# Kernel optimization log

Measured on AMD Instinct MI355X. Metric: run time of the kernel, lower is better.

The kernel has to match this reference:

```python
import jax, jax.numpy as jnp
import numpy as np

N_NODES = 100000
N_EDGES = 1600000
IN_DIM = 128
HID_DIM = 128
OUT_DIM = 2


def sage_conv(x, src, dst, deg_inv, W_l, W_r, b):
    # mean-aggregate neighbor features: messages flow src -> dst
    agg = jax.ops.segment_sum(x[src], dst, num_segments=N_NODES)  # [N, d_in]
    agg = agg * deg_inv[:, None]
    # PyG SAGEConv: out = lin_l(aggr) + lin_r(x); bias only on lin_l
    return agg @ W_l + x @ W_r + b


def setup_inputs() -> dict:
    key = jax.random.key(0)
    ks = jax.random.split(key, 9)
    x = jax.random.normal(ks[0], (N_NODES, IN_DIM), dtype=jnp.float32)
    edge_index = jax.random.randint(ks[1], (2, N_EDGES), 0, N_NODES, dtype=jnp.int64)

    def glorot(k, shape):
        lim = float(np.sqrt(6.0 / (shape[0] + shape[1])))
        return jax.random.uniform(k, shape, jnp.float32, -lim, lim)

    return {
        "x": x,
        "edge_index": edge_index,
        "W1_l": glorot(ks[2], (IN_DIM, HID_DIM)),
        "W1_r": glorot(ks[3], (IN_DIM, HID_DIM)),
        "b1": jnp.zeros((HID_DIM,), jnp.float32),
        "W2_l": glorot(ks[4], (HID_DIM, HID_DIM)),
        "W2_r": glorot(ks[5], (HID_DIM, HID_DIM)),
        "b2": jnp.zeros((HID_DIM,), jnp.float32),
        "W3_l": glorot(ks[6], (HID_DIM, OUT_DIM)),
        "W3_r": glorot(ks[7], (HID_DIM, OUT_DIM)),
        "b3": jnp.zeros((OUT_DIM,), jnp.float32),
    }


def reference(x, edge_index, W1_l, W1_r, b1, W2_l, W2_r, b2, W3_l, W3_r, b3):
    src, dst = edge_index[0], edge_index[1]
    # mean-aggregation normalization: 1/in-degree (clamped to >=1)
    deg = jax.ops.segment_sum(jnp.ones((N_EDGES,), jnp.float32), dst, num_segments=N_NODES)
    deg_inv = 1.0 / jnp.maximum(deg, 1.0)

    h = sage_conv(x, src, dst, deg_inv, W1_l, W1_r, b1)
    h = jax.nn.relu(h)  # dropout is identity in eval mode
    h = sage_conv(h, src, dst, deg_inv, W2_l, W2_r, b2)
    h = jax.nn.relu(h)
    h = sage_conv(h, src, dst, deg_inv, W3_l, W3_r, b3)
    h = jax.nn.relu(h)
    return jax.nn.log_softmax(h, axis=1)
```

## Files before the change

### kernel.cpp

```cpp
#include <hip/hip_runtime.h>
#include <hip/hip_bf16.h>
#include <math.h>

#define DIM 128

typedef __attribute__((ext_vector_type(8))) short bf16x8;
typedef __attribute__((ext_vector_type(4))) float f32x4;

__device__ __forceinline__ ushort f2bf(float f) {
  unsigned u = __float_as_uint(f);
  return (ushort)((u + 0x7FFFu + ((u >> 16) & 1u)) >> 16);
}
__device__ __forceinline__ float bf2f(ushort h) {
  return __uint_as_float(((unsigned)h) << 16);
}

__global__ __launch_bounds__(256) void prep_kernel(
    const int* __restrict__ dst, unsigned* __restrict__ deg, unsigned* __restrict__ rank, int E,
    const float* __restrict__ x, ushort* __restrict__ xh, long total,
    const float* __restrict__ W1l, const float* __restrict__ W1r,
    const float* __restrict__ W2l, const float* __restrict__ W2r,
    ushort* __restrict__ tabs, int H, int C) {
  const int bid = blockIdx.x;
  const int r = bid % 3;
  const int q = bid / 3;
  if (r == 0) {
    if (q < H) {
      int gid = q * 256 + threadIdx.x;
      if (gid < E) rank[gid] = atomicAdd(&deg[dst[gid]], 1u);
    }
    return;
  }
  int id2 = q * 2 + (r - 1);
  if (id2 < C) {
    long i = ((long)id2 * 256 + threadIdx.x) * 4;
    if (i >= total) return;
    float4 v = *(const float4*)(x + i);
    uint2 Hh;
    Hh.x = (unsigned)f2bf(v.x) | ((unsigned)f2bf(v.y) << 16);
    Hh.y = (unsigned)f2bf(v.z) | ((unsigned)f2bf(v.w) << 16);
    *(uint2*)(xh + i) = Hh;
    return;
  }
  id2 -= C;
  if (id2 >= 256) return;
  int m = id2 >> 6;
  const float* W = (m == 0) ? W1l : (m == 1) ? W1r : (m == 2) ? W2l : W2r;
  ushort* Ht = tabs + (size_t)m * 32768;
  ushort* Lt = Ht + 16384;
  int idx = (id2 & 63) * 256 + threadIdx.x;
  int k = idx >> 7, n = idx & 127;
  float v = W[idx];
  ushort h = f2bf(v);
  Ht[n * DIM + k] = h;
  Lt[n * DIM + k] = f2bf(v - bf2f(h));
}

__global__ __launch_bounds__(256) void scan_block_kernel(const unsigned* __restrict__ deg,
                                                         unsigned* __restrict__ excl,
                                                         unsigned* __restrict__ partial,
                                                         float* __restrict__ dinv, int N) {
  __shared__ unsigned s[256];
  int i = blockIdx.x * 256 + threadIdx.x;
  unsigned v = (i < N) ? deg[i] : 0u;
  if (i < N) dinv[i] = 1.0f / fmaxf((float)v, 1.0f);
  s[threadIdx.x] = v;
  __syncthreads();
#pragma unroll
  for (int d = 1; d < 256; d <<= 1) {
    unsigned t = (threadIdx.x >= d) ? s[threadIdx.x - d] : 0u;
    __syncthreads();
    s[threadIdx.x] += t;
    __syncthreads();
  }
  if (i < N) excl[i] = s[threadIdx.x] - v;
  if (threadIdx.x == 255) partial[blockIdx.x] = s[255];
}

__global__ __launch_bounds__(256) void scan_partials_kernel(unsigned* __restrict__ partial, int B) {
  __shared__ unsigned s[256];
  __shared__ unsigned carry;
  if (threadIdx.x == 0) carry = 0u;
  __syncthreads();
  for (int base = 0; base < B; base += 256) {
    int i = base + threadIdx.x;
    unsigned v = (i < B) ? partial[i] : 0u;
    s[threadIdx.x] = v;
    __syncthreads();
#pragma unroll
    for (int d = 1; d < 256; d <<= 1) {
      unsigned t = (threadIdx.x >= d) ? s[threadIdx.x - d] : 0u;
      __syncthreads();
      s[threadIdx.x] += t;
      __syncthreads();
    }
    if (i < B) partial[i] = carry + s[threadIdx.x] - v;
    __syncthreads();
    if (threadIdx.x == 0) carry += s[255];
    __syncthreads();
  }
}

__global__ __launch_bounds__(256) void add_offsets_kernel(const unsigned* __restrict__ excl,
                                                          const unsigned* __restrict__ partial,
                                                          unsigned* __restrict__ off, int N, int E) {
  int i = blockIdx.x * 256 + threadIdx.x;
  if (i < N) off[i] = excl[i] + partial[i >> 8];
  if (i == N) off[N] = (unsigned)E;
}

__global__ __launch_bounds__(256) void csr_fill_kernel(const int* __restrict__ src,
                                                       const int* __restrict__ dst,
                                                       const unsigned* __restrict__ rank,
                                                       const unsigned* __restrict__ off,
                                                       int* __restrict__ csr_src, int E) {
  int e = blockIdx.x * 256 + threadIdx.x;
  if (e >= E) return;
  csr_src[off[dst[e]] + rank[e]] = src[e];
}

__global__ __launch_bounds__(256) void gather_wave_kernel(
    const ushort* __restrict__ featH, const int* __restrict__ csr_src,
    const unsigned* __restrict__ off, const float* __restrict__ dinv,
    ushort* __restrict__ aggH, int N) {
  const int node = (blockIdx.x * 256 + threadIdx.x) >> 6;
  if (node >= N) return;
  const int lane = threadIdx.x & 63;
  const int eslot = lane >> 4;
  const int col = lane & 15;
  const unsigned beg = off[node], end = off[node + 1];
  const ushort* fbase = featH + col * 8;

  float acc[8];
#pragma unroll
  for (int t = 0; t < 8; ++t) acc[t] = 0.f;

  auto accum = [&](int4 v) {
    unsigned w0 = (unsigned)v.x, w1 = (unsigned)v.y, w2 = (unsigned)v.z, w3 = (unsigned)v.w;
    acc[0] += __uint_as_float(w0 << 16);
    acc[1] += __uint_as_float(w0 & 0xFFFF0000u);
    acc[2] += __uint_as_float(w1 << 16);
    acc[3] += __uint_as_float(w1 & 0xFFFF0000u);
    acc[4] += __uint_as_float(w2 << 16);
    acc[5] += __uint_as_float(w2 & 0xFFFF0000u);
    acc[6] += __uint_as_float(w3 << 16);
    acc[7] += __uint_as_float(w3 & 0xFFFF0000u);
  };

  unsigned base = beg;
  for (; base + 16 <= end; base += 16) {
    int s0 = csr_src[base + eslot];
    int s1 = csr_src[base + 4 + eslot];
    int s2 = csr_src[base + 8 + eslot];
    int s3 = csr_src[base + 12 + eslot];
    int4 v0 = *(const int4*)(fbase + (size_t)s0 * DIM);
    int4 v1 = *(const int4*)(fbase + (size_t)s1 * DIM);
    int4 v2 = *(const int4*)(fbase + (size_t)s2 * DIM);
    int4 v3 = *(const int4*)(fbase + (size_t)s3 * DIM);
    accum(v0); accum(v1); accum(v2); accum(v3);
  }
  for (; base + 8 <= end; base += 8) {
    int s0 = csr_src[base + eslot];
    int s1 = csr_src[base + 4 + eslot];
    int4 v0 = *(const int4*)(fbase + (size_t)s0 * DIM);
    int4 v1 = *(const int4*)(fbase + (size_t)s1 * DIM);
    accum(v0); accum(v1);
  }
  for (unsigned e = base + eslot; e < end; e += 4) {
    int s = csr_src[e];
    int4 v = *(const int4*)(fbase + (size_t)s * DIM);
    accum(v);
  }

#pragma unroll
  for (int t = 0; t < 8; ++t) {
    acc[t] += __shfl_xor(acc[t], 32, 64);
    acc[t] += __shfl_xor(acc[t], 16, 64);
  }

  if (eslot == 0) {
    float di = dinv[node];
    unsigned ph[4];
#pragma unroll
    for (int t = 0; t < 4; ++t) {
      ph[t] = (unsigned)f2bf(acc[2 * t] * di) | ((unsigned)f2bf(acc[2 * t + 1] * di) << 16);
    }
    *(int4*)(aggH + (size_t)node * DIM + col * 8) =
        make_int4((int)ph[0], (int)ph[1], (int)ph[2], (int)ph[3]);
  }
}

__global__ __launch_bounds__(256) void sage_mfma_kernel(
    const ushort* __restrict__ aggH, const ushort* xH,
    const ushort* __restrict__ WlH, const ushort* __restrict__ WlL,
    const ushort* __restrict__ WrH, const ushort* __restrict__ WrL,
    const float* __restrict__ bias,
    const float* __restrict__ W3l, const float* __restrict__ W3r,
    ushort* outH, float* __restrict__ y, int N) {
  __shared__ ushort As[128 * 64];
  __shared__ ushort Bs[2 * 128 * 64];

  const int tid = threadIdx.x;
  const int bm = blockIdx.x * 128;
  const int wave = tid >> 6;
  const int lane = tid & 63;
  const int l15 = lane & 15;
  const int quad = lane >> 4;
  const int wm = wave >> 1;
  const int wn = wave & 1;

  f32x4 acc[4][4];
#pragma unroll
  for (int i = 0; i < 4; ++i)
#pragma unroll
    for (int j = 0; j < 4; ++j) acc[i][j] = (f32x4){0.f, 0.f, 0.f, 0.f};

  for (int g = 0; g < 4; ++g) {
    const ushort* Ap = (g < 2) ? aggH : xH;
    const ushort* WH = (g < 2) ? WlH : WrH;
    const ushort* WL = (g < 2) ? WlL : WrL;
    const int kt = (g & 1) << 6;
    __syncthreads();
#pragma unroll
    for (int c = 0; c < 4; ++c) {
      int flat = c * 256 + tid;
      int row = flat >> 3;
      int kg = flat & 7;
      int swz = (kg ^ (row & 7)) << 3;
      int grow = bm + row;
      if (grow >= N) grow = N - 1;
      *(int4*)(&As[row * 64 + swz]) = *(const int4*)(Ap + (size_t)grow * DIM + kt + kg * 8);
    }
#pragma unroll
    for (int c = 0; c < 8; ++c) {
      int flat = c * 256 + tid;
      int tbl = flat >> 10;
      int row = (flat >> 3) & 127;
      int kg = flat & 7;
      int swz = (kg ^ (row & 7)) << 3;
      const ushort* Wp = tbl ? WL : WH;
      *(int4*)(&Bs[tbl * 8192 + row * 64 + swz]) =
          *(const int4*)(Wp + (size_t)row * DIM + kt + kg * 8);
    }
    __syncthreads();
#pragma unroll
    for (int ks = 0; ks < 2; ++ks) {
      bf16x8 af[4], bh[4], bl[4];
      int kg = (ks << 2) + quad;
#pragma unroll
      for (int i = 0; i < 4; ++i) {
        int ar = (wm << 6) + (i << 4) + l15;
        af[i] = *(const bf16x8*)(&As[ar * 64 + ((kg ^ (ar & 7)) << 3)]);
        int br = (wn << 6) + (i << 4) + l15;
        int bo = br * 64 + ((kg ^ (br & 7)) << 3);
        bh[i] = *(const bf16x8*)(&Bs[bo]);
        bl[i] = *(const bf16x8*)(&Bs[8192 + bo]);
      }
#pragma unroll
      for (int i = 0; i < 4; ++i)
#pragma unroll
        for (int j = 0; j < 4; ++j) {
          acc[i][j] = __builtin_amdgcn_mfma_f32_16x16x32_bf16(af[i], bh[j], acc[i][j], 0, 0, 0);
          acc[i][j] = __builtin_amdgcn_mfma_f32_16x16x32_bf16(af[i], bl[j], acc[i][j], 0, 0, 0);
        }
    }
  }

  __syncthreads();
  float* WcF = reinterpret_cast<float*>(As);
  float* YpF = reinterpret_cast<float*>(As) + 512;

  if (W3l) {
    for (int t = tid; t < 512; t += 256) {
      int col = t >> 2, c = t & 3;
      WcF[t] = (c < 2) ? W3l[col * 2 + c] : W3r[col * 2 + (c - 2)];
    }
    __syncthreads();
  }

  float bv[4];
#pragma unroll
  for (int j = 0; j < 4; ++j) bv[j] = bias[(wn << 6) + (j << 4) + l15];

#pragma unroll
  for (int i = 0; i < 4; ++i) {
#pragma unroll
    for (int r = 0; r < 4; ++r) {
      const int rowl = (wm << 6) + (i << 4) + (quad << 2) + r;
      const int grow = bm + rowl;
      float p0 = 0.f, p1 = 0.f, p2 = 0.f, p3 = 0.f;
#pragma unroll
      for (int j = 0; j < 4; ++j) {
        float v = fmaxf(acc[i][j][r] + bv[j], 0.f);
        ushort h = f2bf(v);
        if (grow < N) outH[(size_t)grow * DIM + (wn << 6) + (j << 4) + l15] = h;
        if (W3l) {
          float qv = bf2f(h);
          int col = (wn << 6) + (j << 4) + l15;
          p0 += qv * WcF[col * 4 + 0];
          p1 += qv * WcF[col * 4 + 1];
          p2 += qv * WcF[col * 4 + 2];
          p3 += qv * WcF[col * 4 + 3];
        }
      }
      if (W3l) {
#pragma unroll
        for (int o = 1; o < 16; o <<= 1) {
          p0 += __shfl_xor(p0, o, 64);
          p1 += __shfl_xor(p1, o, 64);
          p2 += __shfl_xor(p2, o, 64);
          p3 += __shfl_xor(p3, o, 64);
        }
        if (l15 == 0) {
          YpF[(rowl * 4 + 0) * 2 + wn] = p0;
          YpF[(rowl * 4 + 1) * 2 + wn] = p1;
          YpF[(rowl * 4 + 2) * 2 + wn] = p2;
          YpF[(rowl * 4 + 3) * 2 + wn] = p3;
        }
      }
    }
  }

  if (W3l) {
    __syncthreads();
    for (int t = tid; t < 512; t += 256) {
      int grow = bm + (t >> 2);
      if (grow < N) y[(size_t)grow * 4 + (t & 3)] = YpF[t * 2 + 0] + YpF[t * 2 + 1];
    }
  }
}

__global__ __launch_bounds__(256) void final3_kernel(const float* __restrict__ y,
                                                     const int* __restrict__ csr_src,
                                                     const unsigned* __restrict__ off,
                                                     const float* __restrict__ dinv,
                                                     const float* __restrict__ b3,
                                                     float* __restrict__ out, int N) {
  int n = blockIdx.x * 256 + threadIdx.x;
  if (n >= N) return;
  unsigned beg = off[n], end = off[n + 1];
  float s0 = 0.f, s1 = 0.f;
  for (unsigned e = beg; e < end; ++e) {
    int s = csr_src[e];
    float2 v = *reinterpret_cast<const float2*>(&y[(size_t)s * 4]);
    s0 += v.x; s1 += v.y;
  }
  float di = dinv[n];
  float o0 = fmaxf(s0 * di + y[(size_t)n * 4 + 2] + b3[0], 0.f);
  float o1 = fmaxf(s1 * di + y[(size_t)n * 4 + 3] + b3[1], 0.f);
  float m = fmaxf(o0, o1);
  float l = m + logf(expf(o0 - m) + expf(o1 - m));
  out[n * 2 + 0] = o0 - l;
  out[n * 2 + 1] = o1 - l;
}

extern "C" void kernel_launch(void* const* d_in, const int* in_sizes, int n_in,
                              void* d_out, int out_size, void* d_ws, size_t ws_size,
                              hipStream_t stream) {
  const float* x   = (const float*)d_in[0];
  const int*   ei  = (const int*)d_in[1];
  const float* W1l = (const float*)d_in[2];
  const float* W1r = (const float*)d_in[3];
  const float* b1  = (const float*)d_in[4];
  const float* W2l = (const float*)d_in[5];
  const float* W2r = (const float*)d_in[6];
  const float* b2  = (const float*)d_in[7];
  const float* W3l = (const float*)d_in[8];
  const float* W3r = (const float*)d_in[9];
  const float* b3  = (const float*)d_in[10];

  const int N = in_sizes[0] / DIM;
  const int E = in_sizes[1] / 2;
  const int* src = ei;
  const int* dst = ei + E;
  const int B = (N + 255) / 256;

  char* ws = (char*)d_ws;
  size_t off_b = 0;
  auto alloc = [&](size_t bytes) {
    void* p = ws + off_b;
    off_b = (off_b + bytes + 255) & ~(size_t)255;
    return p;
  };
  unsigned* deg     = (unsigned*)alloc((size_t)N * 4);
  unsigned* excl    = (unsigned*)alloc((size_t)N * 4);
  unsigned* partial = (unsigned*)alloc((size_t)B * 4);
  unsigned* offs    = (unsigned*)alloc((size_t)(N + 1) * 4);
  unsigned* rank    = (unsigned*)alloc((size_t)E * 4);
  int*      csr_src = (int*)alloc((size_t)E * 4);
  float*    dinv    = (float*)alloc((size_t)N * 4);
  ushort*   xH      = (ushort*)alloc((size_t)N * DIM * 2);
  ushort*   aggH    = (ushort*)alloc((size_t)N * DIM * 2);
  ushort*   wtabs   = (ushort*)alloc((size_t)8 * 16384 * 2);
  float*    y       = (float*)alloc((size_t)N * 4 * 4);

  const int H = (E + 255) / 256;
  const int C = (int)(((size_t)N * DIM / 4 + 255) / 256);
  const int third = (H > (C + 257) / 2) ? H : (C + 257) / 2;
  hipMemsetAsync(deg, 0, (size_t)N * 4, stream);
  prep_kernel<<<third * 3, 256, 0, stream>>>(dst, deg, rank, E, x, xH, (long)N * DIM,
                                             W1l, W1r, W2l, W2r, wtabs, H, C);

  scan_block_kernel<<<B, 256, 0, stream>>>(deg, excl, partial, dinv, N);
  scan_partials_kernel<<<1, 256, 0, stream>>>(partial, B);
  add_offsets_kernel<<<(N + 256) / 256, 256, 0, stream>>>(excl, partial, offs, N, E);
  csr_fill_kernel<<<(E + 255) / 256, 256, 0, stream>>>(src, dst, rank, offs, csr_src, E);

  const ushort* W1lH = wtabs;           const ushort* W1lL = wtabs + 16384;
  const ushort* W1rH = wtabs + 32768;   const ushort* W1rL = wtabs + 49152;
  const ushort* W2lH = wtabs + 65536;   const ushort* W2lL = wtabs + 81920;
  const ushort* W2rH = wtabs + 98304;   const ushort* W2rL = wtabs + 114688;

  const int gemm_grid = (N + 127) / 128;
  const int gather_grid = (N + 3) / 4;

  gather_wave_kernel<<<gather_grid, 256, 0, stream>>>(xH, csr_src, offs, dinv, aggH, N);
  sage_mfma_kernel<<<gemm_grid, 256, 0, stream>>>(aggH, xH, W1lH, W1lL, W1rH, W1rL, b1,
                                                  nullptr, nullptr, xH, nullptr, N);
  gather_wave_kernel<<<gather_grid, 256, 0, stream>>>(xH, csr_src, offs, dinv, aggH, N);
  sage_mfma_kernel<<<gemm_grid, 256, 0, stream>>>(aggH, xH, W2lH, W2lL, W2rH, W2rL, b2,
                                                  W3l, W3r, xH, y, N);
  final3_kernel<<<(N + 255) / 256, 256, 0, stream>>>(y, csr_src, offs, dinv, b3, (float*)d_out, N);
}
```

Baseline: 406.9 us.

## Fuse neighbor gather into the SAGE MFMA GEMM kernel via shared memory

The mean-aggregation gather now runs inside the GEMM kernel. Each 128-row block gathers its own nodes' neighbor sums straight into LDS, so the aggregated feature matrix is no longer written to and reread from global memory. The second layer's hidden output is no longer stored, since only the projected y is used afterwards. Weight staging is split into separate hi/lo passes so shared memory stays at 48 KB, but this adds more barriers. The gather parallelism drops from one wave per node across the whole grid to 32 sequential nodes per wave in only about 782 blocks. That risks latency-bound gathers with poor occupancy, and the gather can no longer overlap with MFMA work in other kernels.

Result: slower. 576.7 us (+41.7%).

```diff
diff --git a/kernel.cpp b/kernel.cpp
--- a/kernel.cpp
+++ b/kernel.cpp
@@ -119,86 +119,16 @@
   csr_src[off[dst[e]] + rank[e]] = src[e];
 }
 
-__global__ __launch_bounds__(256) void gather_wave_kernel(
-    const ushort* __restrict__ featH, const int* __restrict__ csr_src,
+__global__ __launch_bounds__(256) void sage_fused_kernel(
+    const ushort* __restrict__ xin, const int* __restrict__ csr_src,
     const unsigned* __restrict__ off, const float* __restrict__ dinv,
-    ushort* __restrict__ aggH, int N) {
-  const int node = (blockIdx.x * 256 + threadIdx.x) >> 6;
-  if (node >= N) return;
-  const int lane = threadIdx.x & 63;
-  const int eslot = lane >> 4;
-  const int col = lane & 15;
-  const unsigned beg = off[node], end = off[node + 1];
-  const ushort* fbase = featH + col * 8;
-
-  float acc[8];
-#pragma unroll
-  for (int t = 0; t < 8; ++t) acc[t] = 0.f;
-
-  auto accum = [&](int4 v) {
-    unsigned w0 = (unsigned)v.x, w1 = (unsigned)v.y, w2 = (unsigned)v.z, w3 = (unsigned)v.w;
-    acc[0] += __uint_as_float(w0 << 16);
-    acc[1] += __uint_as_float(w0 & 0xFFFF0000u);
-    acc[2] += __uint_as_float(w1 << 16);
-    acc[3] += __uint_as_float(w1 & 0xFFFF0000u);
-    acc[4] += __uint_as_float(w2 << 16);
-    acc[5] += __uint_as_float(w2 & 0xFFFF0000u);
-    acc[6] += __uint_as_float(w3 << 16);
-    acc[7] += __uint_as_float(w3 & 0xFFFF0000u);
-  };
-
-  unsigned base = beg;
-  for (; base + 16 <= end; base += 16) {
-    int s0 = csr_src[base + eslot];
-    int s1 = csr_src[base + 4 + eslot];
-    int s2 = csr_src[base + 8 + eslot];
-    int s3 = csr_src[base + 12 + eslot];
-    int4 v0 = *(const int4*)(fbase + (size_t)s0 * DIM);
-    int4 v1 = *(const int4*)(fbase + (size_t)s1 * DIM);
-    int4 v2 = *(const int4*)(fbase + (size_t)s2 * DIM);
-    int4 v3 = *(const int4*)(fbase + (size_t)s3 * DIM);
-    accum(v0); accum(v1); accum(v2); accum(v3);
-  }
-  for (; base + 8 <= end; base += 8) {
-    int s0 = csr_src[base + eslot];
-    int s1 = csr_src[base + 4 + eslot];
-    int4 v0 = *(const int4*)(fbase + (size_t)s0 * DIM);
-    int4 v1 = *(const int4*)(fbase + (size_t)s1 * DIM);
-    accum(v0); accum(v1);
-  }
-  for (unsigned e = base + eslot; e < end; e += 4) {
-    int s = csr_src[e];
-    int4 v = *(const int4*)(fbase + (size_t)s * DIM);
-    accum(v);
-  }
-
-#pragma unroll
-  for (int t = 0; t < 8; ++t) {
-    acc[t] += __shfl_xor(acc[t], 32, 64);
-    acc[t] += __shfl_xor(acc[t], 16, 64);
-  }
-
-  if (eslot == 0) {
-    float di = dinv[node];
-    unsigned ph[4];
-#pragma unroll
-    for (int t = 0; t < 4; ++t) {
-      ph[t] = (unsigned)f2bf(acc[2 * t] * di) | ((unsigned)f2bf(acc[2 * t + 1] * di) << 16);
-    }
-    *(int4*)(aggH + (size_t)node * DIM + col * 8) =
-        make_int4((int)ph[0], (int)ph[1], (int)ph[2], (int)ph[3]);
-  }
-}
-
-__global__ __launch_bounds__(256) void sage_mfma_kernel(
-    const ushort* __restrict__ aggH, const ushort* xH,
     const ushort* __restrict__ WlH, const ushort* __restrict__ WlL,
     const ushort* __restrict__ WrH, const ushort* __restrict__ WrL,
     const float* __restrict__ bias,
     const float* __restrict__ W3l, const float* __restrict__ W3r,
-    ushort* outH, float* __restrict__ y, int N) {
-  __shared__ ushort As[128 * 64];
-  __shared__ ushort Bs[2 * 128 * 64];
+    ushort* __restrict__ outH, float* __restrict__ y, int N) {
+  __shared__ ushort AsG[128 * 128];
+  __shared__ ushort Bs[128 * 64];
 
   const int tid = threadIdx.x;
   const int bm = blockIdx.x * 128;
@@ -209,66 +139,142 @@
   const int wm = wave >> 1;
   const int wn = wave & 1;
 
+  {
+    const int eslot = lane >> 4;
+    const int col = lane & 15;
+    const ushort* fbase = xin + col * 8;
+    for (int it = 0; it < 32; ++it) {
+      const int nl = it * 4 + wave;
+      int cn = bm + nl;
+      if (cn >= N) cn = N - 1;
+      const unsigned beg = off[cn], end = off[cn + 1];
+      float acc[8];
+#pragma unroll
+      for (int t = 0; t < 8; ++t) acc[t] = 0.f;
+      auto accum = [&](int4 v) {
+        unsigned w0 = (unsigned)v.x, w1 = (unsigned)v.y, w2 = (unsigned)v.z, w3 = (unsigned)v.w;
+        acc[0] += __uint_as_float(w0 << 16);
+        acc[1] += __uint_as_float(w0 & 0xFFFF0000u);
+        acc[2] += __uint_as_float(w1 << 16);
+        acc[3] += __uint_as_float(w1 & 0xFFFF0000u);
+        acc[4] += __uint_as_float(w2 << 16);
+        acc[5] += __uint_as_float(w2 & 0xFFFF0000u);
+        acc[6] += __uint_as_float(w3 << 16);
+        acc[7] += __uint_as_float(w3 & 0xFFFF0000u);
+      };
+      unsigned base = beg;
+      for (; base + 16 <= end; base += 16) {
+        int s0 = csr_src[base + eslot];
+        int s1 = csr_src[base + 4 + eslot];
+        int s2 = csr_src[base + 8 + eslot];
+        int s3 = csr_src[base + 12 + eslot];
+        int4 v0 = *(const int4*)(fbase + (size_t)s0 * DIM);
+        int4 v1 = *(const int4*)(fbase + (size_t)s1 * DIM);
+        int4 v2 = *(const int4*)(fbase + (size_t)s2 * DIM);
+        int4 v3 = *(const int4*)(fbase + (size_t)s3 * DIM);
+        accum(v0); accum(v1); accum(v2); accum(v3);
+      }
+      for (; base + 8 <= end; base += 8) {
+        int s0 = csr_src[base + eslot];
+        int s1 = csr_src[base + 4 + eslot];
+        int4 v0 = *(const int4*)(fbase + (size_t)s0 * DIM);
+        int4 v1 = *(const int4*)(fbase + (size_t)s1 * DIM);
+        accum(v0); accum(v1);
+      }
+      for (unsigned e = base + eslot; e < end; e += 4) {
+        int s = csr_src[e];
+        int4 v = *(const int4*)(fbase + (size_t)s * DIM);
+        accum(v);
+      }
+#pragma unroll
+      for (int t = 0; t < 8; ++t) {
+        acc[t] += __shfl_xor(acc[t], 32, 64);
+        acc[t] += __shfl_xor(acc[t], 16, 64);
+      }
+      if (eslot == 0) {
+        float di = dinv[cn];
+        unsigned ph[4];
+#pragma unroll
+        for (int t = 0; t < 4; ++t)
+          ph[t] = (unsigned)f2bf(acc[2 * t] * di) | ((unsigned)f2bf(acc[2 * t + 1] * di) << 16);
+        int half = col >> 3, kg = col & 7;
+        *(int4*)(&AsG[half * 8192 + nl * 64 + ((kg ^ (nl & 7)) << 3)]) =
+            make_int4((int)ph[0], (int)ph[1], (int)ph[2], (int)ph[3]);
+      }
+    }
+  }
+
   f32x4 acc[4][4];
 #pragma unroll
   for (int i = 0; i < 4; ++i)
 #pragma unroll
     for (int j = 0; j < 4; ++j) acc[i][j] = (f32x4){0.f, 0.f, 0.f, 0.f};
 
-  for (int g = 0; g < 4; ++g) {
-    const ushort* Ap = (g < 2) ? aggH : xH;
-    const ushort* WH = (g < 2) ? WlH : WrH;
-    const ushort* WL = (g < 2) ? WlL : WrL;
-    const int kt = (g & 1) << 6;
-    __syncthreads();
+  auto stageB = [&](const ushort* Wp, int kt) {
 #pragma unroll
     for (int c = 0; c < 4; ++c) {
       int flat = c * 256 + tid;
-      int row = flat >> 3;
-      int kg = flat & 7;
-      int swz = (kg ^ (row & 7)) << 3;
+      int row = flat >> 3, kg = flat & 7;
+      *(int4*)(&Bs[row * 64 + ((kg ^ (row & 7)) << 3)]) =
+          *(const int4*)(Wp + (size_t)row * DIM + kt + kg * 8);
+    }
+  };
+  auto mfma32 = [&](const ushort* Ab) {
+#pragma unroll
+    for (int ks = 0; ks < 2; ++ks) {
+      bf16x8 af[4], bfr[4];
+      int kg = (ks << 2) + quad;
+#pragma unroll
+      for (int i = 0; i < 4; ++i) {
+        int ar = (wm << 6) + (i << 4) + l15;
+        af[i] = *(const bf16x8*)(&Ab[ar * 64 + ((kg ^ (ar & 7)) << 3)]);
+        int br = (wn << 6) + (i << 4) + l15;
+        bfr[i] = *(const bf16x8*)(&Bs[br * 64 + ((kg ^ (br & 7)) << 3)]);
+      }
+#pragma unroll
+      for (int i = 0; i < 4; ++i)
+#pragma unroll
+        for (int j = 0; j < 4; ++j)
+          acc[i][j] = __builtin_amdgcn_mfma_f32_16x16x32_bf16(af[i], bfr[j], acc[i][j], 0, 0, 0);
+    }
+  };
+
+  __syncthreads();
+
+  for (int t = 0; t < 2; ++t) {
+    const ushort* Wp = t ? WlL : WlH;
+    for (int ktb = 0; ktb < 2; ++ktb) {
+      if (t || ktb) __syncthreads();
+      stageB(Wp, ktb << 6);
+      __syncthreads();
+      mfma32(&AsG[ktb * 8192]);
+    }
+  }
+
+  ushort* Ax = AsG;
+  for (int ktb = 0; ktb < 2; ++ktb) {
+    __syncthreads();
+#pragma unroll
+    for (int c = 0; c < 4; ++c) {
+      int flat = c * 256 + tid;
+      int row = flat >> 3, kg = flat & 7;
       int grow = bm + row;
       if (grow >= N) grow = N - 1;
-      *(int4*)(&As[row * 64 + swz]) = *(const int4*)(Ap + (size_t)grow * DIM + kt + kg * 8);
-    }
-#pragma unroll
-    for (int c = 0; c < 8; ++c) {
-      int flat = c * 256 + tid;
-      int tbl = flat >> 10;
-      int row = (flat >> 3) & 127;
-      int kg = flat & 7;
-      int swz = (kg ^ (row & 7)) << 3;
-      const ushort* Wp = tbl ? WL : WH;
-      *(int4*)(&Bs[tbl * 8192 + row * 64 + swz]) =
-          *(const int4*)(Wp + (size_t)row * DIM + kt + kg * 8);
-    }
-    __syncthreads();
-#pragma unroll
-    for (int ks = 0; ks < 2; ++ks) {
-      bf16x8 af[4], bh[4], bl[4];
-      int kg = (ks << 2) + quad;
-#pragma unroll
-      for (int i = 0; i < 4; ++i) {
-        int ar = (wm << 6) + (i << 4) + l15;
-        af[i] = *(const bf16x8*)(&As[ar * 64 + ((kg ^ (ar & 7)) << 3)]);
-        int br = (wn << 6) + (i << 4) + l15;
-        int bo = br * 64 + ((kg ^ (br & 7)) << 3);
-        bh[i] = *(const bf16x8*)(&Bs[bo]);
-        bl[i] = *(const bf16x8*)(&Bs[8192 + bo]);
-      }
-#pragma unroll
-      for (int i = 0; i < 4; ++i)
-#pragma unroll
-        for (int j = 0; j < 4; ++j) {
-          acc[i][j] = __builtin_amdgcn_mfma_f32_16x16x32_bf16(af[i], bh[j], acc[i][j], 0, 0, 0);
-          acc[i][j] = __builtin_amdgcn_mfma_f32_16x16x32_bf16(af[i], bl[j], acc[i][j], 0, 0, 0);
-        }
-    }
+      *(int4*)(&Ax[row * 64 + ((kg ^ (row & 7)) << 3)]) =
+          *(const int4*)(xin + (size_t)grow * DIM + (ktb << 6) + kg * 8);
+    }
+    stageB(WrH, ktb << 6);
+    __syncthreads();
+    mfma32(Ax);
+    __syncthreads();
+    stageB(WrL, ktb << 6);
+    __syncthreads();
+    mfma32(Ax);
   }
 
   __syncthreads();
-  float* WcF = reinterpret_cast<float*>(As);
-  float* YpF = reinterpret_cast<float*>(As) + 512;
+  float* WcF = reinterpret_cast<float*>(AsG);
+  float* YpF = reinterpret_cast<float*>(AsG) + 512;
 
   if (W3l) {
     for (int t = tid; t < 512; t += 256) {
@@ -293,7 +299,7 @@
       for (int j = 0; j < 4; ++j) {
         float v = fmaxf(acc[i][j][r] + bv[j], 0.f);
         ushort h = f2bf(v);
-        if (grow < N) outH[(size_t)grow * DIM + (wn << 6) + (j << 4) + l15] = h;
+        if (outH && grow < N) outH[(size_t)grow * DIM + (wn << 6) + (j << 4) + l15] = h;
         if (W3l) {
           float qv = bf2f(h);
           int col = (wn << 6) + (j << 4) + l15;
@@ -390,7 +396,7 @@
   int*      csr_src = (int*)alloc((size_t)E * 4);
   float*    dinv    = (float*)alloc((size_t)N * 4);
   ushort*   xH      = (ushort*)alloc((size_t)N * DIM * 2);
-  ushort*   aggH    = (ushort*)alloc((size_t)N * DIM * 2);
+  ushort*   hbuf    = (ushort*)alloc((size_t)N * DIM * 2);
   ushort*   wtabs   = (ushort*)alloc((size_t)8 * 16384 * 2);
   float*    y       = (float*)alloc((size_t)N * 4 * 4);
 
@@ -412,13 +418,12 @@
   const ushort* W2rH = wtabs + 98304;   const ushort* W2rL = wtabs + 114688;
 
   const int gemm_grid = (N + 127) / 128;
-  const int gather_grid = (N + 3) / 4;
-
-  gather_wave_kernel<<<gather_grid, 256, 0, stream>>>(xH, csr_src, offs, dinv, aggH, N);
-  sage_mfma_kernel<<<gemm_grid, 256, 0, stream>>>(aggH, xH, W1lH, W1lL, W1rH, W1rL, b1,
-                                                  nullptr, nullptr, xH, nullptr, N);
-  gather_wave_kernel<<<gather_grid, 256, 0, stream>>>(xH, csr_src, offs, dinv, aggH, N);
-  sage_mfma_kernel<<<gemm_grid, 256, 0, stream>>>(aggH, xH, W2lH, W2lL, W2rH, W2rL, b2,
-                                                  W3l, W3r, xH, y, N);
+
+  sage_fused_kernel<<<gemm_grid, 256, 0, stream>>>(xH, csr_src, offs, dinv,
+                                                   W1lH, W1lL, W1rH, W1rL, b1,
+                                                   nullptr, nullptr, hbuf, nullptr, N);
+  sage_fused_kernel<<<gemm_grid, 256, 0, stream>>>(hbuf, csr_src, offs, dinv,
+                                                   W2lH, W2lL, W2rH, W2rL, b2,
+                                                   W3l, W3r, nullptr, y, N);
   final3_kernel<<<(N + 255) / 256, 256, 0, stream>>>(y, csr_src, offs, dinv, b3, (float*)d_out, N);
 }
```

## Overlap layer-1 root GEMM with CSR fill in one fused launch

Applied to the files above, without the earlier changes.

Merges the offset computation and CSR fill into one kernel, and gives every sixth block the job of computing x@W1_r (the layer-1 self term) with MFMA. The blocks are interleaved so that bandwidth-bound scatter work and compute-bound GEMM work run side by side. The layer-1 GEMM then only handles the aggregated half and adds the precomputed bf16 self term, while layer 2 no longer writes outH. The cost is an extra N×128 bf16 buffer written and read back, plus an intermediate bf16 rounding of the self term.

Result: slower. 432.7 us (+6.3%).

```diff
diff --git a/kernel.cpp b/kernel.cpp
--- a/kernel.cpp
+++ b/kernel.cpp
@@ -101,22 +101,101 @@
   }
 }
 
-__global__ __launch_bounds__(256) void add_offsets_kernel(const unsigned* __restrict__ excl,
-                                                          const unsigned* __restrict__ partial,
-                                                          unsigned* __restrict__ off, int N, int E) {
-  int i = blockIdx.x * 256 + threadIdx.x;
-  if (i < N) off[i] = excl[i] + partial[i >> 8];
-  if (i == N) off[N] = (unsigned)E;
-}
-
-__global__ __launch_bounds__(256) void csr_fill_kernel(const int* __restrict__ src,
-                                                       const int* __restrict__ dst,
-                                                       const unsigned* __restrict__ rank,
-                                                       const unsigned* __restrict__ off,
-                                                       int* __restrict__ csr_src, int E) {
-  int e = blockIdx.x * 256 + threadIdx.x;
-  if (e >= E) return;
-  csr_src[off[dst[e]] + rank[e]] = src[e];
+__global__ __launch_bounds__(256) void fill_linr_kernel(
+    const int* __restrict__ src, const int* __restrict__ dst,
+    const unsigned* __restrict__ rank, const unsigned* __restrict__ excl,
+    const unsigned* __restrict__ partial, unsigned* __restrict__ off,
+    int* __restrict__ csr_src, int E, int N,
+    const ushort* __restrict__ xH, const ushort* __restrict__ WrH,
+    const ushort* __restrict__ WrL, ushort* __restrict__ hr, int G, int A) {
+  __shared__ ushort As[128 * 64];
+  __shared__ ushort Bs[128 * 64];
+
+  const int bid = blockIdx.x;
+  const int r = bid % 6;
+  const int q = bid / 6;
+  const int tid = threadIdx.x;
+
+  if (r < 5) {
+    int fid = q * 5 + r;
+    int e = fid * 256 + tid;
+    if (e < E) {
+      int d = dst[e];
+      csr_src[excl[d] + partial[d >> 8] + rank[e]] = src[e];
+    }
+    return;
+  }
+  if (q >= G) {
+    int qa = q - G;
+    if (qa < A) {
+      int i = qa * 256 + tid;
+      if (i < N) off[i] = excl[i] + partial[i >> 8];
+      if (i == N) off[N] = (unsigned)E;
+    }
+    return;
+  }
+
+  const int bm = q * 128;
+  const int wave = tid >> 6;
+  const int lane = tid & 63;
+  const int l15 = lane & 15;
+  const int quad = lane >> 4;
+  const int wm = wave >> 1;
+  const int wn = wave & 1;
+
+  f32x4 acc[4][4];
+#pragma unroll
+  for (int i = 0; i < 4; ++i)
+#pragma unroll
+    for (int j = 0; j < 4; ++j) acc[i][j] = (f32x4){0.f, 0.f, 0.f, 0.f};
+
+  for (int t = 0; t < 2; ++t) {
+    const ushort* Wp = t ? WrL : WrH;
+    for (int ktb = 0; ktb < 2; ++ktb) {
+      if (t || ktb) __syncthreads();
+      const int kt = ktb << 6;
+#pragma unroll
+      for (int c = 0; c < 4; ++c) {
+        int flat = c * 256 + tid;
+        int row = flat >> 3, kg = flat & 7;
+        int swz = (kg ^ (row & 7)) << 3;
+        int grow = bm + row;
+        if (grow >= N) grow = N - 1;
+        *(int4*)(&As[row * 64 + swz]) = *(const int4*)(xH + (size_t)grow * DIM + kt + kg * 8);
+        *(int4*)(&Bs[row * 64 + swz]) = *(const int4*)(Wp + (size_t)row * DIM + kt + kg * 8);
+      }
+      __syncthreads();
+#pragma unroll
+      for (int ks = 0; ks < 2; ++ks) {
+        bf16x8 af[4], bfr[4];
+        int kg = (ks << 2) + quad;
+#pragma unroll
+        for (int i = 0; i < 4; ++i) {
+          int ar = (wm << 6) + (i << 4) + l15;
+          af[i] = *(const bf16x8*)(&As[ar * 64 + ((kg ^ (ar & 7)) << 3)]);
+          int br = (wn << 6) + (i << 4) + l15;
+          bfr[i] = *(const bf16x8*)(&Bs[br * 64 + ((kg ^ (br & 7)) << 3)]);
+        }
+#pragma unroll
+        for (int i = 0; i < 4; ++i)
+#pragma unroll
+          for (int j = 0; j < 4; ++j)
+            acc[i][j] = __builtin_amdgcn_mfma_f32_16x16x32_bf16(af[i], bfr[j], acc[i][j], 0, 0, 0);
+      }
+    }
+  }
+
+#pragma unroll
+  for (int i = 0; i < 4; ++i)
+#pragma unroll
+    for (int rr = 0; rr < 4; ++rr) {
+      int grow = bm + (wm << 6) + (i << 4) + (quad << 2) + rr;
+      if (grow < N) {
+#pragma unroll
+        for (int j = 0; j < 4; ++j)
+          hr[(size_t)grow * DIM + (wn << 6) + (j << 4) + l15] = f2bf(acc[i][j][rr]);
+      }
+    }
 }
 
 __global__ __launch_bounds__(256) void gather_wave_kernel(
@@ -196,7 +275,8 @@
     const ushort* __restrict__ WrH, const ushort* __restrict__ WrL,
     const float* __restrict__ bias,
     const float* __restrict__ W3l, const float* __restrict__ W3r,
-    ushort* outH, float* __restrict__ y, int N) {
+    const ushort* __restrict__ addin,
+    ushort* __restrict__ outH, float* __restrict__ y, int N) {
   __shared__ ushort As[128 * 64];
   __shared__ ushort Bs[2 * 128 * 64];
 
@@ -215,7 +295,8 @@
 #pragma unroll
     for (int j = 0; j < 4; ++j) acc[i][j] = (f32x4){0.f, 0.f, 0.f, 0.f};
 
-  for (int g = 0; g < 4; ++g) {
+  const int ng = addin ? 2 : 4;
+  for (int g = 0; g < ng; ++g) {
     const ushort* Ap = (g < 2) ? aggH : xH;
     const ushort* WH = (g < 2) ? WlH : WrH;
     const ushort* WL = (g < 2) ? WlL : WrL;
@@ -291,12 +372,14 @@
       float p0 = 0.f, p1 = 0.f, p2 = 0.f, p3 = 0.f;
 #pragma unroll
       for (int j = 0; j < 4; ++j) {
-        float v = fmaxf(acc[i][j][r] + bv[j], 0.f);
+        int col = (wn << 6) + (j << 4) + l15;
+        float v = acc[i][j][r] + bv[j];
+        if (addin && grow < N) v += bf2f(addin[(size_t)grow * DIM + col]);
+        v = fmaxf(v, 0.f);
         ushort h = f2bf(v);
-        if (grow < N) outH[(size_t)grow * DIM + (wn << 6) + (j << 4) + l15] = h;
+        if (outH && grow < N) outH[(size_t)grow * DIM + col] = h;
         if (W3l) {
           float qv = bf2f(h);
-          int col = (wn << 6) + (j << 4) + l15;
           p0 += qv * WcF[col * 4 + 0];
           p1 += qv * WcF[col * 4 + 1];
           p2 += qv * WcF[col * 4 + 2];
@@ -390,6 +473,7 @@
   int*      csr_src = (int*)alloc((size_t)E * 4);
   float*    dinv    = (float*)alloc((size_t)N * 4);
   ushort*   xH      = (ushort*)alloc((size_t)N * DIM * 2);
+  ushort*   hbuf    = (ushort*)alloc((size_t)N * DIM * 2);
   ushort*   aggH    = (ushort*)alloc((size_t)N * DIM * 2);
   ushort*   wtabs   = (ushort*)alloc((size_t)8 * 16384 * 2);
   float*    y       = (float*)alloc((size_t)N * 4 * 4);
@@ -403,22 +487,30 @@
 
   scan_block_kernel<<<B, 256, 0, stream>>>(deg, excl, partial, dinv, N);
   scan_partials_kernel<<<1, 256, 0, stream>>>(partial, B);
-  add_offsets_kernel<<<(N + 256) / 256, 256, 0, stream>>>(excl, partial, offs, N, E);
-  csr_fill_kernel<<<(E + 255) / 256, 256, 0, stream>>>(src, dst, rank, offs, csr_src, E);
 
   const ushort* W1lH = wtabs;           const ushort* W1lL = wtabs + 16384;
   const ushort* W1rH = wtabs + 32768;   const ushort* W1rL = wtabs + 49152;
   const ushort* W2lH = wtabs + 65536;   const ushort* W2lL = wtabs + 81920;
   const ushort* W2rH = wtabs + 98304;   const ushort* W2rL = wtabs + 114688;
 
-  const int gemm_grid = (N + 127) / 128;
+  const int G = (N + 127) / 128;
+  const int A = (N + 256) / 256;
+
+  {
+    const int F = (E + 255) / 256;
+    int Q = (F + 4) / 5;
+    if (Q < G + A) Q = G + A;
+    fill_linr_kernel<<<Q * 6, 256, 0, stream>>>(src, dst, rank, excl, partial, offs, csr_src,
+                                                E, N, xH, W1rH, W1rL, hbuf, G, A);
+  }
+
   const int gather_grid = (N + 3) / 4;
 
   gather_wave_kernel<<<gather_grid, 256, 0, stream>>>(xH, csr_src, offs, dinv, aggH, N);
-  sage_mfma_kernel<<<gemm_grid, 256, 0, stream>>>(aggH, xH, W1lH, W1lL, W1rH, W1rL, b1,
-                                                  nullptr, nullptr, xH, nullptr, N);
+  sage_mfma_kernel<<<G, 256, 0, stream>>>(aggH, nullptr, W1lH, W1lL, nullptr, nullptr, b1,
+                                          nullptr, nullptr, hbuf, xH, nullptr, N);
   gather_wave_kernel<<<gather_grid, 256, 0, stream>>>(xH, csr_src, offs, dinv, aggH, N);
-  sage_mfma_kernel<<<gemm_grid, 256, 0, stream>>>(aggH, xH, W2lH, W2lL, W2rH, W2rL, b2,
-                                                  W3l, W3r, xH, y, N);
+  sage_mfma_kernel<<<G, 256, 0, stream>>>(aggH, xH, W2lH, W2lL, W2rH, W2rL, b2,
+                                          W3l, W3r, nullptr, nullptr, y, N);
   final3_kernel<<<(N + 255) / 256, 256, 0, stream>>>(y, csr_src, offs, dinv, b3, (float*)d_out, N);
 }
```

## Drop bf16 hi/lo weight split and skip unused layer-2 hidden output store

Applied to the files above, without the earlier changes.

Weights are now stored as a single bf16 table instead of a high/low bf16 pair, which halves the MFMA count, the weight loads into shared memory and the LDS footprint in the GEMM kernel. The second GEMM no longer writes its bf16 hidden output, since only the projected y values are consumed afterwards. This lowers weight precision to plain bf16, which may increase error relative to the fp32 reference.

After: 397.5 us. 1.02x faster.

```diff
diff --git a/kernel.cpp b/kernel.cpp
--- a/kernel.cpp
+++ b/kernel.cpp
@@ -46,14 +46,10 @@
   if (id2 >= 256) return;
   int m = id2 >> 6;
   const float* W = (m == 0) ? W1l : (m == 1) ? W1r : (m == 2) ? W2l : W2r;
-  ushort* Ht = tabs + (size_t)m * 32768;
-  ushort* Lt = Ht + 16384;
+  ushort* Ht = tabs + (size_t)m * 16384;
   int idx = (id2 & 63) * 256 + threadIdx.x;
   int k = idx >> 7, n = idx & 127;
-  float v = W[idx];
-  ushort h = f2bf(v);
-  Ht[n * DIM + k] = h;
-  Lt[n * DIM + k] = f2bf(v - bf2f(h));
+  Ht[n * DIM + k] = f2bf(W[idx]);
 }
 
 __global__ __launch_bounds__(256) void scan_block_kernel(const unsigned* __restrict__ deg,
@@ -192,13 +188,12 @@
 
 __global__ __launch_bounds__(256) void sage_mfma_kernel(
     const ushort* __restrict__ aggH, const ushort* xH,
-    const ushort* __restrict__ WlH, const ushort* __restrict__ WlL,
-    const ushort* __restrict__ WrH, const ushort* __restrict__ WrL,
+    const ushort* __restrict__ WlH, const ushort* __restrict__ WrH,
     const float* __restrict__ bias,
     const float* __restrict__ W3l, const float* __restrict__ W3r,
-    ushort* outH, float* __restrict__ y, int N) {
+    ushort* __restrict__ outH, float* __restrict__ y, int N) {
   __shared__ ushort As[128 * 64];
-  __shared__ ushort Bs[2 * 128 * 64];
+  __shared__ ushort Bs[128 * 64];
 
   const int tid = threadIdx.x;
   const int bm = blockIdx.x * 128;
@@ -217,8 +212,7 @@
 
   for (int g = 0; g < 4; ++g) {
     const ushort* Ap = (g < 2) ? aggH : xH;
-    const ushort* WH = (g < 2) ? WlH : WrH;
-    const ushort* WL = (g < 2) ? WlL : WrL;
+    const ushort* Wp = (g < 2) ? WlH : WrH;
     const int kt = (g & 1) << 6;
     __syncthreads();
 #pragma unroll
@@ -230,39 +224,25 @@
       int grow = bm + row;
       if (grow >= N) grow = N - 1;
       *(int4*)(&As[row * 64 + swz]) = *(const int4*)(Ap + (size_t)grow * DIM + kt + kg * 8);
-    }
-#pragma unroll
-    for (int c = 0; c < 8; ++c) {
-      int flat = c * 256 + tid;
-      int tbl = flat >> 10;
-      int row = (flat >> 3) & 127;
-      int kg = flat & 7;
-      int swz = (kg ^ (row & 7)) << 3;
-      const ushort* Wp = tbl ? WL : WH;
-      *(int4*)(&Bs[tbl * 8192 + row * 64 + swz]) =
-          *(const int4*)(Wp + (size_t)row * DIM + kt + kg * 8);
+      *(int4*)(&Bs[row * 64 + swz]) = *(const int4*)(Wp + (size_t)row * DIM + kt + kg * 8);
     }
     __syncthreads();
 #pragma unroll
     for (int ks = 0; ks < 2; ++ks) {
-      bf16x8 af[4], bh[4], bl[4];
+      bf16x8 af[4], bfr[4];
       int kg = (ks << 2) + quad;
 #pragma unroll
       for (int i = 0; i < 4; ++i) {
         int ar = (wm << 6) + (i << 4) + l15;
         af[i] = *(const bf16x8*)(&As[ar * 64 + ((kg ^ (ar & 7)) << 3)]);
         int br = (wn << 6) + (i << 4) + l15;
-        int bo = br * 64 + ((kg ^ (br & 7)) << 3);
-        bh[i] = *(const bf16x8*)(&Bs[bo]);
-        bl[i] = *(const bf16x8*)(&Bs[8192 + bo]);
+        bfr[i] = *(const bf16x8*)(&Bs[br * 64 + ((kg ^ (br & 7)) << 3)]);
       }
 #pragma unroll
       for (int i = 0; i < 4; ++i)
 #pragma unroll
-        for (int j = 0; j < 4; ++j) {
-          acc[i][j] = __builtin_amdgcn_mfma_f32_16x16x32_bf16(af[i], bh[j], acc[i][j], 0, 0, 0);
-          acc[i][j] = __builtin_amdgcn_mfma_f32_16x16x32_bf16(af[i], bl[j], acc[i][j], 0, 0, 0);
-        }
+        for (int j = 0; j < 4; ++j)
+          acc[i][j] = __builtin_amdgcn_mfma_f32_16x16x32_bf16(af[i], bfr[j], acc[i][j], 0, 0, 0);
     }
   }
 
@@ -291,12 +271,12 @@
       float p0 = 0.f, p1 = 0.f, p2 = 0.f, p3 = 0.f;
 #pragma unroll
       for (int j = 0; j < 4; ++j) {
+        int col = (wn << 6) + (j << 4) + l15;
         float v = fmaxf(acc[i][j][r] + bv[j], 0.f);
         ushort h = f2bf(v);
-        if (grow < N) outH[(size_t)grow * DIM + (wn << 6) + (j << 4) + l15] = h;
+        if (outH && grow < N) outH[(size_t)grow * DIM + col] = h;
         if (W3l) {
           float qv = bf2f(h);
-          int col = (wn << 6) + (j << 4) + l15;
           p0 += qv * WcF[col * 4 + 0];
           p1 += qv * WcF[col * 4 + 1];
           p2 += qv * WcF[col * 4 + 2];
@@ -391,7 +371,7 @@
   float*    dinv    = (float*)alloc((size_t)N * 4);
   ushort*   xH      = (ushort*)alloc((size_t)N * DIM * 2);
   ushort*   aggH    = (ushort*)alloc((size_t)N * DIM * 2);
-  ushort*   wtabs   = (ushort*)alloc((size_t)8 * 16384 * 2);
+  ushort*   wtabs   = (ushort*)alloc((size_t)4 * 16384 * 2);
   float*    y       = (float*)alloc((size_t)N * 4 * 4);
 
   const int H = (E + 255) / 256;
@@ -406,19 +386,19 @@
   add_offsets_kernel<<<(N + 256) / 256, 256, 0, stream>>>(excl, partial, offs, N, E);
   csr_fill_kernel<<<(E + 255) / 256, 256, 0, stream>>>(src, dst, rank, offs, csr_src, E);
 
-  const ushort* W1lH = wtabs;           const ushort* W1lL = wtabs + 16384;
-  const ushort* W1rH = wtabs + 32768;   const ushort* W1rL = wtabs + 49152;
-  const ushort* W2lH = wtabs + 65536;   const ushort* W2lL = wtabs + 81920;
-  const ushort* W2rH = wtabs + 98304;   const ushort* W2rL = wtabs + 114688;
-
-  const int gemm_grid = (N + 127) / 128;
+  const ushort* W1lH = wtabs;
+  const ushort* W1rH = wtabs + 16384;
+  const ushort* W2lH = wtabs + 32768;
+  const ushort* W2rH = wtabs + 49152;
+
+  const int G = (N + 127) / 128;
   const int gather_grid = (N + 3) / 4;
 
   gather_wave_kernel<<<gather_grid, 256, 0, stream>>>(xH, csr_src, offs, dinv, aggH, N);
-  sage_mfma_kernel<<<gemm_grid, 256, 0, stream>>>(aggH, xH, W1lH, W1lL, W1rH, W1rL, b1,
-                                                  nullptr, nullptr, xH, nullptr, N);
+  sage_mfma_kernel<<<G, 256, 0, stream>>>(aggH, xH, W1lH, W1rH, b1,
+                                          nullptr, nullptr, xH, nullptr, N);
   gather_wave_kernel<<<gather_grid, 256, 0, stream>>>(xH, csr_src, offs, dinv, aggH, N);
-  sage_mfma_kernel<<<gemm_grid, 256, 0, stream>>>(aggH, xH, W2lH, W2lL, W2rH, W2rL, b2,
-                                                  W3l, W3r, xH, y, N);
+  sage_mfma_kernel<<<G, 256, 0, stream>>>(aggH, xH, W2lH, W2rH, b2,
+                                          W3l, W3r, nullptr, y, N);
   final3_kernel<<<(N + 255) / 256, 256, 0, stream>>>(y, csr_src, offs, dinv, b3, (float*)d_out, N);
 }
```
